# Kernel tuning notes

Measured on AMD Instinct MI355X. Metric: run time of the kernel, lower is better.

The kernel has to match this reference:

```python
import jax, jax.numpy as jnp
import numpy as np

N = 8192          # total proposals
D_IN = 256 * 7 * 7  # 12544
HID = 1024
C = 3


def setup_inputs() -> dict:
    key = jax.random.key(0)
    ks = jax.random.split(key, 9)
    s_in = 1.0 / np.sqrt(D_IN)
    s_h = 1.0 / np.sqrt(HID)
    return {
        "feature_vectors": jax.random.normal(ks[0], (N, D_IN), dtype=jnp.float32),
        "W1": jax.random.uniform(ks[1], (D_IN, HID), jnp.float32, -s_in, s_in),
        "b1": jax.random.uniform(ks[2], (HID,), jnp.float32, -s_in, s_in),
        "W2": jax.random.uniform(ks[3], (HID, HID), jnp.float32, -s_h, s_h),
        "b2": jax.random.uniform(ks[4], (HID,), jnp.float32, -s_h, s_h),
        "Wc": jax.random.uniform(ks[5], (HID, C + 1), jnp.float32, -s_h, s_h),
        "bc": jax.random.uniform(ks[6], (C + 1,), jnp.float32, -s_h, s_h),
        "Wr": jax.random.uniform(ks[7], (HID, 4 * C), jnp.float32, -s_h, s_h),
        "br": jax.random.uniform(ks[8], (4 * C,), jnp.float32, -s_h, s_h),
    }


def reference(feature_vectors, W1, b1, W2, b2, Wc, bc, Wr, br):
    # intermediate: Linear -> Linear -> ReLU (note: no ReLU between the two Linears,
    # matching the original nn.Sequential ordering)
    h = feature_vectors @ W1 + b1          # [N, 1024]
    h = h @ W2 + b2                        # [N, 1024]
    h = jax.nn.relu(h)
    class_logits = jax.nn.softmax(h @ Wc + bc, axis=-1)  # [N, C+1]
    box_pred = h @ Wr + br                  # [N, 4C]
    return class_logits, box_pred
```

## Files before the change

kernel.cpp:

```cpp
#include <hip/hip_runtime.h>
#include <hip/hip_bf16.h>
#include <stdint.h>

using u16 = unsigned short;
using u32 = unsigned int;

typedef __attribute__((ext_vector_type(8))) short short8;
typedef __attribute__((ext_vector_type(4))) float floatx4;

__device__ __forceinline__ u16 f2bf(float f) {
  __hip_bfloat16 h = __float2bfloat16(f);
  return *reinterpret_cast<u16*>(&h);
}

__device__ __forceinline__ void gl_lds16(const void* g, void* l) {
  __builtin_amdgcn_global_load_lds((const __attribute__((address_space(1))) void*)g,
                                   (__attribute__((address_space(3))) void*)l, 16, 0, 0);
}

__global__ __launch_bounds__(256)
void transpose_to_bf16(const float* __restrict__ in, u16* __restrict__ out,
                       int R, int Cc) {
  __shared__ float tile[32][33];
  int c0 = blockIdx.x * 32;
  int r0 = blockIdx.y * 32;
  int tx = threadIdx.x;
  int ty = threadIdx.y;
#pragma unroll
  for (int i = 0; i < 32; i += 8)
    tile[ty + i][tx] = in[(size_t)(r0 + ty + i) * Cc + c0 + tx];
  __syncthreads();
#pragma unroll
  for (int i = 0; i < 32; i += 8)
    out[(size_t)(c0 + ty + i) * R + r0 + tx] = f2bf(tile[tx][ty + i]);
}

__global__ __launch_bounds__(256)
void cvt_bf16(const float4* __restrict__ in, uint2* __restrict__ out, int n4) {
  int i = blockIdx.x * 256 + threadIdx.x;
  if (i >= n4) return;
  float4 v = in[i];
  u32 lo = (u32)f2bf(v.x) | ((u32)f2bf(v.y) << 16);
  u32 hi = (u32)f2bf(v.z) | ((u32)f2bf(v.w) << 16);
  out[i] = make_uint2(lo, hi);
}

constexpr int BM = 128, BN = 128, BK = 32;

template <bool A_BF16, bool RELU>
__global__ __launch_bounds__(256, 3)
void gemm_bt(const void* __restrict__ Aip, const u16* __restrict__ BT,
             const float* __restrict__ bias, u16* __restrict__ C,
             int M, int N, int K) {
  __shared__ __align__(16) u16 As[BM * BK];
  __shared__ __align__(16) u16 Bs[BN * BK];
  const int tid  = threadIdx.x;
  const int lane = tid & 63;
  const int wave = tid >> 6;
  const int m0 = blockIdx.y * BM;
  const int n0 = blockIdx.x * BN;
  const int wm = (wave & 1) * 64;
  const int wn = (wave >> 1) * 64;
  const int row = lane & 15;
  const int kq  = lane >> 4;

  floatx4 acc[4][4] = {};

  int a_off[4], b_off[4];
#pragma unroll
  for (int t = 0; t < 4; ++t) {
    int mr = wm + t * 16 + row;
    a_off[t] = mr * BK + ((kq ^ ((mr >> 1) & 3)) * 8);
    int nr = wn + t * 16 + row;
    b_off[t] = nr * BK + ((kq ^ ((nr >> 1) & 3)) * 8);
  }

  const u16* bptr[2];
  int b_lds[2];
#pragma unroll
  for (int it = 0; it < 2; ++it) {
    int c = it * 256 + tid;
    int nrow = c >> 2;
    int kc = ((c & 3) ^ ((nrow >> 1) & 3)) * 8;
    bptr[it] = BT + (size_t)(n0 + nrow) * K + kc;
    b_lds[it] = (it * 256 + wave * 64) * 8;
  }

  const u16* aptrB[2];
  int a_ldsB[2];
  const float* aptrF[4];
  int a_stF[4];
  if constexpr (A_BF16) {
    const u16* A = (const u16*)Aip;
#pragma unroll
    for (int it = 0; it < 2; ++it) {
      int c = it * 256 + tid;
      int mrow = c >> 2;
      int kc = ((c & 3) ^ ((mrow >> 1) & 3)) * 8;
      aptrB[it] = A + (size_t)(m0 + mrow) * K + kc;
      a_ldsB[it] = (it * 256 + wave * 64) * 8;
    }
  } else {
    const float* A = (const float*)Aip;
#pragma unroll
    for (int it = 0; it < 4; ++it) {
      int idx = it * 256 + tid;
      int mrow = idx >> 3;
      int kc = (idx & 7) * 4;
      aptrF[it] = A + (size_t)(m0 + mrow) * K + kc;
      int chunk = kc >> 3, half = (kc >> 2) & 1;
      int sc = chunk ^ ((mrow >> 1) & 3);
      a_stF[it] = mrow * BK + sc * 8 + half * 4;
    }
  }

  for (int k0 = 0; k0 < K; k0 += BK) {
    __syncthreads();
    if constexpr (A_BF16) {
#pragma unroll
      for (int it = 0; it < 2; ++it)
        gl_lds16(aptrB[it] + k0, &As[a_ldsB[it]]);
    } else {
#pragma unroll
      for (int it = 0; it < 4; ++it) {
        float4 v = *(const float4*)(aptrF[it] + k0);
        u32 lo = (u32)f2bf(v.x) | ((u32)f2bf(v.y) << 16);
        u32 hi = (u32)f2bf(v.z) | ((u32)f2bf(v.w) << 16);
        *(uint2*)&As[a_stF[it]] = make_uint2(lo, hi);
      }
    }
#pragma unroll
    for (int it = 0; it < 2; ++it)
      gl_lds16(bptr[it] + k0, &Bs[b_lds[it]]);
    __syncthreads();

    short8 a[4], b[4];
#pragma unroll
    for (int t = 0; t < 4; ++t) {
      a[t] = *(const short8*)&As[a_off[t]];
      b[t] = *(const short8*)&Bs[b_off[t]];
    }
#pragma unroll
    for (int mt = 0; mt < 4; ++mt)
#pragma unroll
      for (int nt = 0; nt < 4; ++nt)
        acc[mt][nt] = __builtin_amdgcn_mfma_f32_16x16x32_bf16(
            a[mt], b[nt], acc[mt][nt], 0, 0, 0);
  }

  const int ccol = row;
  const int crow = kq * 4;
#pragma unroll
  for (int mt = 0; mt < 4; ++mt) {
#pragma unroll
    for (int nt = 0; nt < 4; ++nt) {
      int gm = m0 + wm + mt * 16 + crow;
      int gn = n0 + wn + nt * 16 + ccol;
      float bv = bias[gn];
#pragma unroll
      for (int r = 0; r < 4; ++r) {
        float v = acc[mt][nt][r] + bv;
        if (RELU) v = fmaxf(v, 0.f);
        C[(size_t)(gm + r) * N + gn] = f2bf(v);
      }
    }
  }
}

constexpr int A_BUF  = 256 * 64;
constexpr int B_BUF  = 128 * 64;
constexpr int B_BASE = 3 * A_BUF;
constexpr int LDS_BYTES = (3 * A_BUF + 3 * B_BUF) * 2;

#define MM(i, j, va, vb) \
  acc[i][j] = __builtin_amdgcn_mfma_f32_16x16x32_bf16(va, vb, acc[i][j], 0, 0, 0)
#define MEMF() asm volatile("" ::: "memory")
#define BAR() do { MEMF(); __builtin_amdgcn_s_barrier(); MEMF(); } while (0)
#define STAGE_AH(h, bufo) \
  do { gl_lds16(apt[h][0], lds + (bufo) + adst[h][0]); apt[h][0] += 64; \
       gl_lds16(apt[h][1], lds + (bufo) + adst[h][1]); apt[h][1] += 64; } while (0)
#define STAGE_BH(h, bufo) \
  do { gl_lds16(bpt[h], lds + (bufo) + bdst[h]); bpt[h] += 64; } while (0)

template <bool RELU>
__global__ __launch_bounds__(512, 2)
void gemm256(const u16* __restrict__ A, const u16* __restrict__ BT,
             const float* __restrict__ bias, u16* __restrict__ C,
             int N, int K) {
  extern __shared__ u16 lds[];
  const int tid  = threadIdx.x;
  const int lane = tid & 63;
  const int wave = tid >> 6;
  const int wm = wave >> 1;
  const int wn = wave & 1;
  const int row = lane & 15;
  const int kq  = lane >> 4;
  const int sw  = lane & 7;

  const int orig = blockIdx.y * 8 + blockIdx.x;
  const int rr = ((orig & 7) << 5) | (orig >> 3);
  const int n0 = (rr & 7) * 128;
  const int m0 = (rr >> 3) * 256;

  const int o0 = ((kq) ^ sw) * 8;
  const int o1 = ((4 | kq) ^ sw) * 8;
  const int ar0 = (wm * 64 + row) * 64;
  const int ar1 = ar0 + 16 * 64;
  const int ar2 = ar0 + 32 * 64;
  const int ar3 = ar0 + 48 * 64;
  const int br0 = (wn * 64 + row) * 64;
  const int br1 = br0 + 16 * 64;
  const int br2 = br0 + 32 * 64;
  const int br3 = br0 + 48 * 64;

  const u16* apt[2][2];
  int adst[2][2];
#pragma unroll
  for (int h = 0; h < 2; ++h)
#pragma unroll
    for (int L = 0; L < 2; ++L) {
      int i = L * 512 + tid;
      int rg = h * 128 + (i >> 3);
      int c = i & 7;
      apt[h][L] = A + (size_t)(m0 + rg) * K + ((c ^ (rg & 7)) * 8);
      adst[h][L] = h * 8192 + L * 4096 + wave * 512;
    }
  const u16* bpt[2];
  int bdst[2];
#pragma unroll
  for (int h = 0; h < 2; ++h) {
    int rg = h * 64 + (tid >> 3);
    int c = tid & 7;
    bpt[h] = BT + (size_t)(n0 + rg) * K + ((c ^ (rg & 7)) * 8);
    bdst[h] = B_BASE + h * 4096 + wave * 512;
  }

  STAGE_AH(0, 0);      STAGE_AH(1, 0);      STAGE_BH(0, 0);     STAGE_BH(1, 0);
  STAGE_AH(0, A_BUF);  STAGE_AH(1, A_BUF);  STAGE_BH(0, B_BUF); STAGE_BH(1, B_BUF);
  asm volatile("s_waitcnt vmcnt(6)" ::: "memory");
  BAR();

  floatx4 acc[4][4] = {};
  int cb = 0, sb = 2;
  const int NT = K >> 6;
  for (int T = 0; T < NT; ++T) {
    const bool st = (T + 2 < NT);
    const u16* Ac = lds + cb * A_BUF;
    const u16* Bc = lds + B_BASE + cb * B_BUF;
    const int sA = sb * A_BUF;
    const int sB = sb * B_BUF;

    short8 a0k0, a0k1, a1k0, a1k1, a2k0, a2k1, a3k0, a3k1;
    short8 b0k0, b0k1, b1k0, b1k1, b2k0, b2k1, b3k0, b3k1;

    a0k0 = *(const short8*)(Ac + ar0 + o0);
    a0k1 = *(const short8*)(Ac + ar0 + o1);
    a1k0 = *(const short8*)(Ac + ar1 + o0);
    a1k1 = *(const short8*)(Ac + ar1 + o1);
    b0k0 = *(const short8*)(Bc + br0 + o0);
    b0k1 = *(const short8*)(Bc + br0 + o1);
    b1k0 = *(const short8*)(Bc + br1 + o0);
    b1k1 = *(const short8*)(Bc + br1 + o1);
    if (st) STAGE_AH(0, sA);
    BAR();
    __builtin_amdgcn_s_setprio(1);
    MM(0, 0, a0k0, b0k0); MM(0, 1, a0k0, b1k0);
    MM(1, 0, a1k0, b0k0); MM(1, 1, a1k0, b1k0);
    MM(0, 0, a0k1, b0k1); MM(0, 1, a0k1, b1k1);
    MM(1, 0, a1k1, b0k1); MM(1, 1, a1k1, b1k1);
    __builtin_amdgcn_s_setprio(0);
    BAR();

    b2k0 = *(const short8*)(Bc + br2 + o0);
    b2k1 = *(const short8*)(Bc + br2 + o1);
    b3k0 = *(const short8*)(Bc + br3 + o0);
    b3k1 = *(const short8*)(Bc + br3 + o1);
    if (st) STAGE_AH(1, sA);
    BAR();
    __builtin_amdgcn_s_setprio(1);
    MM(0, 2, a0k0, b2k0); MM(0, 3, a0k0, b3k0);
    MM(1, 2, a1k0, b2k0); MM(1, 3, a1k0, b3k0);
    MM(0, 2, a0k1, b2k1); MM(0, 3, a0k1, b3k1);
    MM(1, 2, a1k1, b2k1); MM(1, 3, a1k1, b3k1);
    __builtin_amdgcn_s_setprio(0);
    BAR();

    a2k0 = *(const short8*)(Ac + ar2 + o0);
    a2k1 = *(const short8*)(Ac + ar2 + o1);
    a3k0 = *(const short8*)(Ac + ar3 + o0);
    a3k1 = *(const short8*)(Ac + ar3 + o1);
    if (st) STAGE_BH(0, sB);
    BAR();
    __builtin_amdgcn_s_setprio(1);
    MM(2, 2, a2k0, b2k0); MM(2, 3, a2k0, b3k0);
    MM(3, 2, a3k0, b2k0); MM(3, 3, a3k0, b3k0);
    MM(2, 2, a2k1, b2k1); MM(2, 3, a2k1, b3k1);
    MM(3, 2, a3k1, b2k1); MM(3, 3, a3k1, b3k1);
    __builtin_amdgcn_s_setprio(0);
    BAR();

    if (st) STAGE_BH(1, sB);
    BAR();
    __builtin_amdgcn_s_setprio(1);
    MM(2, 0, a2k0, b0k0); MM(2, 1, a2k0, b1k0);
    MM(3, 0, a3k0, b0k0); MM(3, 1, a3k0, b1k0);
    MM(2, 0, a2k1, b0k1); MM(2, 1, a2k1, b1k1);
    MM(3, 0, a3k1, b0k1); MM(3, 1, a3k1, b1k1);
    __builtin_amdgcn_s_setprio(0);
    if (st) asm volatile("s_waitcnt vmcnt(6)" ::: "memory");
    else    asm volatile("s_waitcnt vmcnt(0)" ::: "memory");
    BAR();

    cb = (cb == 2) ? 0 : cb + 1;
    sb = (sb == 2) ? 0 : sb + 1;
  }

#pragma unroll
  for (int mt = 0; mt < 4; ++mt) {
#pragma unroll
    for (int nt = 0; nt < 4; ++nt) {
      int gm = m0 + wm * 64 + mt * 16 + kq * 4;
      int gn = n0 + wn * 64 + nt * 16 + row;
      float bv = bias[gn];
#pragma unroll
      for (int r = 0; r < 4; ++r) {
        float v = acc[mt][nt][r] + bv;
        if (RELU) v = fmaxf(v, 0.f);
        C[(size_t)(gm + r) * N + gn] = f2bf(v);
      }
    }
  }
}

__device__ __forceinline__ float wave_sum(float v) {
#pragma unroll
  for (int m = 32; m >= 1; m >>= 1) v += __shfl_xor(v, m, 64);
  return v;
}

__global__ __launch_bounds__(64)
void head_kernel(const u16* __restrict__ H, const float* __restrict__ Wc,
                 const float* __restrict__ bc, const float* __restrict__ Wr,
                 const float* __restrict__ br, float* __restrict__ out) {
  const int rowi = blockIdx.x;
  const int lane = threadIdx.x;
  const u16* h = H + (size_t)rowi * 1024 + lane * 16;
  uint4 p0 = *(const uint4*)h;
  uint4 p1 = *(const uint4*)(h + 8);
  u32 w[8] = {p0.x, p0.y, p0.z, p0.w, p1.x, p1.y, p1.z, p1.w};
  float x[16];
#pragma unroll
  for (int i = 0; i < 8; ++i) {
    union { u32 u; float f; } lo, hi;
    lo.u = w[i] << 16;
    hi.u = w[i] & 0xffff0000u;
    x[2 * i] = lo.f;
    x[2 * i + 1] = hi.f;
  }
  float ac[4] = {};
  float ar[12] = {};
  const int kbase = lane * 16;
#pragma unroll
  for (int j = 0; j < 16; ++j) {
    float xv = x[j];
    const float* wc = Wc + (size_t)(kbase + j) * 4;
#pragma unroll
    for (int c = 0; c < 4; ++c) ac[c] = fmaf(xv, wc[c], ac[c]);
    const float* wr = Wr + (size_t)(kbase + j) * 12;
#pragma unroll
    for (int r = 0; r < 12; ++r) ar[r] = fmaf(xv, wr[r], ar[r]);
  }
#pragma unroll
  for (int c = 0; c < 4; ++c) ac[c] = wave_sum(ac[c]);
#pragma unroll
  for (int r = 0; r < 12; ++r) ar[r] = wave_sum(ar[r]);

  if (lane == 0) {
    float lg[4], mx = -1e30f;
#pragma unroll
    for (int c = 0; c < 4; ++c) { lg[c] = ac[c] + bc[c]; mx = fmaxf(mx, lg[c]); }
    float s = 0.f;
#pragma unroll
    for (int c = 0; c < 4; ++c) { lg[c] = __expf(lg[c] - mx); s += lg[c]; }
    float inv = 1.f / s;
#pragma unroll
    for (int c = 0; c < 4; ++c) out[(size_t)rowi * 4 + c] = lg[c] * inv;
    float* ob = out + 8192 * 4;
#pragma unroll
    for (int r = 0; r < 12; ++r) ob[(size_t)rowi * 12 + r] = ar[r] + br[r];
  }
}

extern "C" void kernel_launch(void* const* d_in, const int* in_sizes, int n_in,
                              void* d_out, int out_size, void* d_ws, size_t ws_size,
                              hipStream_t stream) {
  const float* X  = (const float*)d_in[0];
  const float* W1 = (const float*)d_in[1];
  const float* b1 = (const float*)d_in[2];
  const float* W2 = (const float*)d_in[3];
  const float* b2 = (const float*)d_in[4];
  const float* Wc = (const float*)d_in[5];
  const float* bc = (const float*)d_in[6];
  const float* Wr = (const float*)d_in[7];
  const float* br = (const float*)d_in[8];

  constexpr int NP = 8192, DIN = 12544, HID = 1024;
  char* ws = (char*)d_ws;
  u16* W1T = (u16*)ws;
  u16* W2T = (u16*)(ws + (size_t)HID * DIN * 2);
  u16* H1  = (u16*)((char*)W2T + (size_t)HID * HID * 2);
  u16* Hb  = H1 + (size_t)NP * HID;
  u16* Xb  = Hb + (size_t)NP * HID;
  size_t need_base = (size_t)HID * DIN * 2 + (size_t)HID * HID * 2 +
                     2 * (size_t)NP * HID * 2;
  bool use_xbf = ws_size >= need_base + (size_t)NP * DIN * 2;

  static bool s_attr = false;
  if (!s_attr) {
    hipFuncSetAttribute(reinterpret_cast<const void*>(gemm256<false>),
                        hipFuncAttributeMaxDynamicSharedMemorySize, LDS_BYTES);
    hipFuncSetAttribute(reinterpret_cast<const void*>(gemm256<true>),
                        hipFuncAttributeMaxDynamicSharedMemorySize, LDS_BYTES);
    s_attr = true;
  }

  transpose_to_bf16<<<dim3(HID / 32, DIN / 32), dim3(32, 8), 0, stream>>>(W1, W1T, DIN, HID);
  transpose_to_bf16<<<dim3(HID / 32, HID / 32), dim3(32, 8), 0, stream>>>(W2, W2T, HID, HID);

  if (use_xbf) {
    int n4 = NP * DIN / 4;
    cvt_bf16<<<(n4 + 255) / 256, 256, 0, stream>>>((const float4*)X, (uint2*)Xb, n4);
    gemm256<false><<<dim3(8, NP / 256), 512, LDS_BYTES, stream>>>(
        Xb, W1T, b1, H1, HID, DIN);
  } else {
    gemm_bt<false, false><<<dim3(HID / BN, NP / BM), 256, 0, stream>>>(
        X, W1T, b1, H1, NP, HID, DIN);
  }
  gemm256<true><<<dim3(8, NP / 256), 512, LDS_BYTES, stream>>>(
      H1, W2T, b2, Hb, HID, HID);
  head_kernel<<<NP, 64, 0, stream>>>(Hb, Wc, bc, Wr, br, (float*)d_out);
}
```

Measured before the change: 877.1 us.

## Fuse fp32-to-bf16 conversion of X into first GEMM's load pipeline

Replaces the separate cvt_bf16 pass over X plus the bf16 GEMM with a new 256x128-tile kernel that loads fp32 X through registers, converts it to bf16 and writes it into double-buffered LDS while MFMAs run. This removes a full write and re-read of the 8192x12544 bf16 copy of X. The cost is that the A operand now goes through registers instead of direct global-to-LDS loads, and the kernel uses two LDS stages instead of three. The head kernel also packs four rows per 256-thread block to cut the block count.

```diff
diff --git a/kernel.cpp b/kernel.cpp
--- a/kernel.cpp
+++ b/kernel.cpp
@@ -35,147 +35,16 @@
     out[(size_t)(c0 + ty + i) * R + r0 + tx] = f2bf(tile[tx][ty + i]);
 }
 
-__global__ __launch_bounds__(256)
-void cvt_bf16(const float4* __restrict__ in, uint2* __restrict__ out, int n4) {
-  int i = blockIdx.x * 256 + threadIdx.x;
-  if (i >= n4) return;
-  float4 v = in[i];
-  u32 lo = (u32)f2bf(v.x) | ((u32)f2bf(v.y) << 16);
-  u32 hi = (u32)f2bf(v.z) | ((u32)f2bf(v.w) << 16);
-  out[i] = make_uint2(lo, hi);
-}
-
-constexpr int BM = 128, BN = 128, BK = 32;
-
-template <bool A_BF16, bool RELU>
-__global__ __launch_bounds__(256, 3)
-void gemm_bt(const void* __restrict__ Aip, const u16* __restrict__ BT,
-             const float* __restrict__ bias, u16* __restrict__ C,
-             int M, int N, int K) {
-  __shared__ __align__(16) u16 As[BM * BK];
-  __shared__ __align__(16) u16 Bs[BN * BK];
-  const int tid  = threadIdx.x;
-  const int lane = tid & 63;
-  const int wave = tid >> 6;
-  const int m0 = blockIdx.y * BM;
-  const int n0 = blockIdx.x * BN;
-  const int wm = (wave & 1) * 64;
-  const int wn = (wave >> 1) * 64;
-  const int row = lane & 15;
-  const int kq  = lane >> 4;
-
-  floatx4 acc[4][4] = {};
-
-  int a_off[4], b_off[4];
-#pragma unroll
-  for (int t = 0; t < 4; ++t) {
-    int mr = wm + t * 16 + row;
-    a_off[t] = mr * BK + ((kq ^ ((mr >> 1) & 3)) * 8);
-    int nr = wn + t * 16 + row;
-    b_off[t] = nr * BK + ((kq ^ ((nr >> 1) & 3)) * 8);
-  }
-
-  const u16* bptr[2];
-  int b_lds[2];
-#pragma unroll
-  for (int it = 0; it < 2; ++it) {
-    int c = it * 256 + tid;
-    int nrow = c >> 2;
-    int kc = ((c & 3) ^ ((nrow >> 1) & 3)) * 8;
-    bptr[it] = BT + (size_t)(n0 + nrow) * K + kc;
-    b_lds[it] = (it * 256 + wave * 64) * 8;
-  }
-
-  const u16* aptrB[2];
-  int a_ldsB[2];
-  const float* aptrF[4];
-  int a_stF[4];
-  if constexpr (A_BF16) {
-    const u16* A = (const u16*)Aip;
-#pragma unroll
-    for (int it = 0; it < 2; ++it) {
-      int c = it * 256 + tid;
-      int mrow = c >> 2;
-      int kc = ((c & 3) ^ ((mrow >> 1) & 3)) * 8;
-      aptrB[it] = A + (size_t)(m0 + mrow) * K + kc;
-      a_ldsB[it] = (it * 256 + wave * 64) * 8;
-    }
-  } else {
-    const float* A = (const float*)Aip;
-#pragma unroll
-    for (int it = 0; it < 4; ++it) {
-      int idx = it * 256 + tid;
-      int mrow = idx >> 3;
-      int kc = (idx & 7) * 4;
-      aptrF[it] = A + (size_t)(m0 + mrow) * K + kc;
-      int chunk = kc >> 3, half = (kc >> 2) & 1;
-      int sc = chunk ^ ((mrow >> 1) & 3);
-      a_stF[it] = mrow * BK + sc * 8 + half * 4;
-    }
-  }
-
-  for (int k0 = 0; k0 < K; k0 += BK) {
-    __syncthreads();
-    if constexpr (A_BF16) {
-#pragma unroll
-      for (int it = 0; it < 2; ++it)
-        gl_lds16(aptrB[it] + k0, &As[a_ldsB[it]]);
-    } else {
-#pragma unroll
-      for (int it = 0; it < 4; ++it) {
-        float4 v = *(const float4*)(aptrF[it] + k0);
-        u32 lo = (u32)f2bf(v.x) | ((u32)f2bf(v.y) << 16);
-        u32 hi = (u32)f2bf(v.z) | ((u32)f2bf(v.w) << 16);
-        *(uint2*)&As[a_stF[it]] = make_uint2(lo, hi);
-      }
-    }
-#pragma unroll
-    for (int it = 0; it < 2; ++it)
-      gl_lds16(bptr[it] + k0, &Bs[b_lds[it]]);
-    __syncthreads();
-
-    short8 a[4], b[4];
-#pragma unroll
-    for (int t = 0; t < 4; ++t) {
-      a[t] = *(const short8*)&As[a_off[t]];
-      b[t] = *(const short8*)&Bs[b_off[t]];
-    }
-#pragma unroll
-    for (int mt = 0; mt < 4; ++mt)
-#pragma unroll
-      for (int nt = 0; nt < 4; ++nt)
-        acc[mt][nt] = __builtin_amdgcn_mfma_f32_16x16x32_bf16(
-            a[mt], b[nt], acc[mt][nt], 0, 0, 0);
-  }
-
-  const int ccol = row;
-  const int crow = kq * 4;
-#pragma unroll
-  for (int mt = 0; mt < 4; ++mt) {
-#pragma unroll
-    for (int nt = 0; nt < 4; ++nt) {
-      int gm = m0 + wm + mt * 16 + crow;
-      int gn = n0 + wn + nt * 16 + ccol;
-      float bv = bias[gn];
-#pragma unroll
-      for (int r = 0; r < 4; ++r) {
-        float v = acc[mt][nt][r] + bv;
-        if (RELU) v = fmaxf(v, 0.f);
-        C[(size_t)(gm + r) * N + gn] = f2bf(v);
-      }
-    }
-  }
-}
+#define MM(i, j, va, vb) \
+  acc[i][j] = __builtin_amdgcn_mfma_f32_16x16x32_bf16(va, vb, acc[i][j], 0, 0, 0)
+#define MEMF() asm volatile("" ::: "memory")
+#define BAR() do { MEMF(); __builtin_amdgcn_s_barrier(); MEMF(); } while (0)
 
 constexpr int A_BUF  = 256 * 64;
 constexpr int B_BUF  = 128 * 64;
 constexpr int B_BASE = 3 * A_BUF;
 constexpr int LDS_BYTES = (3 * A_BUF + 3 * B_BUF) * 2;
 
-#define MM(i, j, va, vb) \
-  acc[i][j] = __builtin_amdgcn_mfma_f32_16x16x32_bf16(va, vb, acc[i][j], 0, 0, 0)
-#define MEMF() asm volatile("" ::: "memory")
-#define BAR() do { MEMF(); __builtin_amdgcn_s_barrier(); MEMF(); } while (0)
 #define STAGE_AH(h, bufo) \
   do { gl_lds16(apt[h][0], lds + (bufo) + adst[h][0]); apt[h][0] += 64; \
        gl_lds16(apt[h][1], lds + (bufo) + adst[h][1]); apt[h][1] += 64; } while (0)
@@ -332,18 +201,194 @@
   }
 }
 
+constexpr int FA_BUF  = 256 * 64;
+constexpr int FB_BUF  = 128 * 64;
+constexpr int FB_BASE = 2 * FA_BUF;
+constexpr int LDS_BYTES_F = (2 * FA_BUF + 2 * FB_BUF) * 2;
+
+__device__ __forceinline__ void cvtw64(u16* dst, float4 v) {
+  u32 lo = (u32)f2bf(v.x) | ((u32)f2bf(v.y) << 16);
+  u32 hi = (u32)f2bf(v.z) | ((u32)f2bf(v.w) << 16);
+  *(uint2*)dst = make_uint2(lo, hi);
+}
+
+__global__ __launch_bounds__(512, 2)
+void gemm256F(const float* __restrict__ A, const u16* __restrict__ BT,
+              const float* __restrict__ bias, u16* __restrict__ C,
+              int N, int K) {
+  extern __shared__ u16 lds[];
+  const int tid  = threadIdx.x;
+  const int lane = tid & 63;
+  const int wave = tid >> 6;
+  const int wm = wave >> 1;
+  const int wn = wave & 1;
+  const int row = lane & 15;
+  const int kq  = lane >> 4;
+  const int sw  = lane & 7;
+
+  const int orig = blockIdx.y * 8 + blockIdx.x;
+  const int rr = ((orig & 7) << 5) | (orig >> 3);
+  const int n0 = (rr & 7) * 128;
+  const int m0 = (rr >> 3) * 256;
+
+  const int o0 = ((kq) ^ sw) * 8;
+  const int o1 = ((4 | kq) ^ sw) * 8;
+  const int ar0 = (wm * 64 + row) * 64;
+  const int ar1 = ar0 + 16 * 64;
+  const int ar2 = ar0 + 32 * 64;
+  const int ar3 = ar0 + 48 * 64;
+  const int br0 = (wn * 64 + row) * 64;
+  const int br1 = br0 + 16 * 64;
+  const int br2 = br0 + 32 * 64;
+  const int br3 = br0 + 48 * 64;
+
+  const u16* bpt[2];
+  int bdst[2];
+#pragma unroll
+  for (int h = 0; h < 2; ++h) {
+    int rg = h * 64 + (tid >> 3);
+    int c = tid & 7;
+    bpt[h] = BT + (size_t)(n0 + rg) * K + ((c ^ (rg & 7)) * 8);
+    bdst[h] = h * 4096 + wave * 512;
+  }
+
+  const float* aFk = A + (size_t)(m0 + (tid >> 4)) * K + (tid & 15) * 4;
+  const int r0t = tid >> 4;
+  const int c4 = tid & 15;
+  const int adst0 = r0t * 64 + (((c4 >> 1) ^ (r0t & 7)) * 8) + (c4 & 1) * 4;
+
+  float4 rA[2][4];
+
+#define FSTAGE_ISSUE(nB_)                                              \
+  do {                                                                 \
+    MEMF();                                                            \
+    gl_lds16(bpt[0], lds + (nB_) + bdst[0]); bpt[0] += 64;             \
+    gl_lds16(bpt[1], lds + (nB_) + bdst[1]); bpt[1] += 64;             \
+    MEMF();                                                            \
+    _Pragma("unroll")                                                  \
+    for (int h = 0; h < 2; ++h)                                        \
+      _Pragma("unroll")                                                \
+      for (int i = 0; i < 4; ++i)                                      \
+        rA[h][i] = *(const float4*)(aFk + (size_t)(h * 128 + i * 32) * K); \
+    aFk += 64;                                                         \
+    MEMF();                                                            \
+  } while (0)
+
+#define FSTAGE_WRITE(nA_)                                              \
+  do {                                                                 \
+    asm volatile("s_waitcnt vmcnt(4)" ::: "memory");                   \
+    _Pragma("unroll")                                                  \
+    for (int i = 0; i < 4; ++i)                                        \
+      cvtw64(lds + (nA_) + adst0 + (i * 32) * 64, rA[0][i]);           \
+    asm volatile("s_waitcnt vmcnt(0)" ::: "memory");                   \
+    _Pragma("unroll")                                                  \
+    for (int i = 0; i < 4; ++i)                                        \
+      cvtw64(lds + (nA_) + adst0 + ((128 + i * 32)) * 64, rA[1][i]);   \
+  } while (0)
+
+  FSTAGE_ISSUE(FB_BASE + 0);
+  FSTAGE_WRITE(0);
+  asm volatile("s_waitcnt lgkmcnt(0)" ::: "memory");
+  BAR();
+
+  floatx4 acc[4][4] = {};
+  const int NT = K >> 6;
+  for (int T = 0; T < NT; ++T) {
+    const int cur = T & 1;
+    const bool st = (T + 1 < NT);
+    const u16* Ac = lds + cur * FA_BUF;
+    const u16* Bc = lds + FB_BASE + cur * FB_BUF;
+    const int nA = (cur ^ 1) * FA_BUF;
+    const int nB = FB_BASE + (cur ^ 1) * FB_BUF;
+
+    short8 a0k0, a0k1, a1k0, a1k1, a2k0, a2k1, a3k0, a3k1;
+    short8 b0k0, b0k1, b1k0, b1k1, b2k0, b2k1, b3k0, b3k1;
+
+    a0k0 = *(const short8*)(Ac + ar0 + o0);
+    a0k1 = *(const short8*)(Ac + ar0 + o1);
+    a1k0 = *(const short8*)(Ac + ar1 + o0);
+    a1k1 = *(const short8*)(Ac + ar1 + o1);
+    b0k0 = *(const short8*)(Bc + br0 + o0);
+    b0k1 = *(const short8*)(Bc + br0 + o1);
+    b1k0 = *(const short8*)(Bc + br1 + o0);
+    b1k1 = *(const short8*)(Bc + br1 + o1);
+    if (st) FSTAGE_ISSUE(nB);
+    BAR();
+    __builtin_amdgcn_s_setprio(1);
+    MM(0, 0, a0k0, b0k0); MM(0, 1, a0k0, b1k0);
+    MM(1, 0, a1k0, b0k0); MM(1, 1, a1k0, b1k0);
+    MM(0, 0, a0k1, b0k1); MM(0, 1, a0k1, b1k1);
+    MM(1, 0, a1k1, b0k1); MM(1, 1, a1k1, b1k1);
+    __builtin_amdgcn_s_setprio(0);
+    BAR();
+
+    b2k0 = *(const short8*)(Bc + br2 + o0);
+    b2k1 = *(const short8*)(Bc + br2 + o1);
+    b3k0 = *(const short8*)(Bc + br3 + o0);
+    b3k1 = *(const short8*)(Bc + br3 + o1);
+    BAR();
+    __builtin_amdgcn_s_setprio(1);
+    MM(0, 2, a0k0, b2k0); MM(0, 3, a0k0, b3k0);
+    MM(1, 2, a1k0, b2k0); MM(1, 3, a1k0, b3k0);
+    MM(0, 2, a0k1, b2k1); MM(0, 3, a0k1, b3k1);
+    MM(1, 2, a1k1, b2k1); MM(1, 3, a1k1, b3k1);
+    __builtin_amdgcn_s_setprio(0);
+    BAR();
+
+    a2k0 = *(const short8*)(Ac + ar2 + o0);
+    a2k1 = *(const short8*)(Ac + ar2 + o1);
+    a3k0 = *(const short8*)(Ac + ar3 + o0);
+    a3k1 = *(const short8*)(Ac + ar3 + o1);
+    BAR();
+    __builtin_amdgcn_s_setprio(1);
+    MM(2, 2, a2k0, b2k0); MM(2, 3, a2k0, b3k0);
+    MM(3, 2, a3k0, b2k0); MM(3, 3, a3k0, b3k0);
+    MM(2, 2, a2k1, b2k1); MM(2, 3, a2k1, b3k1);
+    MM(3, 2, a3k1, b2k1); MM(3, 3, a3k1, b3k1);
+    __builtin_amdgcn_s_setprio(0);
+    BAR();
+
+    if (st) FSTAGE_WRITE(nA);
+    __builtin_amdgcn_s_setprio(1);
+    MM(2, 0, a2k0, b0k0); MM(2, 1, a2k0, b1k0);
+    MM(3, 0, a3k0, b0k0); MM(3, 1, a3k0, b1k0);
+    MM(2, 0, a2k1, b0k1); MM(2, 1, a2k1, b1k1);
+    MM(3, 0, a3k1, b0k1); MM(3, 1, a3k1, b1k1);
+    __builtin_amdgcn_s_setprio(0);
+    asm volatile("s_waitcnt lgkmcnt(0)" ::: "memory");
+    BAR();
+  }
+
+#pragma unroll
+  for (int mt = 0; mt < 4; ++mt) {
+#pragma unroll
+    for (int nt = 0; nt < 4; ++nt) {
+      int gm = m0 + wm * 64 + mt * 16 + kq * 4;
+      int gn = n0 + wn * 64 + nt * 16 + row;
+      float bv = bias[gn];
+#pragma unroll
+      for (int r = 0; r < 4; ++r) {
+        float v = acc[mt][nt][r] + bv;
+        C[(size_t)(gm + r) * N + gn] = f2bf(v);
+      }
+    }
+  }
+#undef FSTAGE_ISSUE
+#undef FSTAGE_WRITE
+}
+
 __device__ __forceinline__ float wave_sum(float v) {
 #pragma unroll
   for (int m = 32; m >= 1; m >>= 1) v += __shfl_xor(v, m, 64);
   return v;
 }
 
-__global__ __launch_bounds__(64)
+__global__ __launch_bounds__(256)
 void head_kernel(const u16* __restrict__ H, const float* __restrict__ Wc,
                  const float* __restrict__ bc, const float* __restrict__ Wr,
                  const float* __restrict__ br, float* __restrict__ out) {
-  const int rowi = blockIdx.x;
-  const int lane = threadIdx.x;
+  const int rowi = blockIdx.x * 4 + (threadIdx.x >> 6);
+  const int lane = threadIdx.x & 63;
   const u16* h = H + (size_t)rowi * 1024 + lane * 16;
   uint4 p0 = *(const uint4*)h;
   uint4 p1 = *(const uint4*)(h + 8);
@@ -410,15 +455,12 @@
   u16* W2T = (u16*)(ws + (size_t)HID * DIN * 2);
   u16* H1  = (u16*)((char*)W2T + (size_t)HID * HID * 2);
   u16* Hb  = H1 + (size_t)NP * HID;
-  u16* Xb  = Hb + (size_t)NP * HID;
-  size_t need_base = (size_t)HID * DIN * 2 + (size_t)HID * HID * 2 +
-                     2 * (size_t)NP * HID * 2;
-  bool use_xbf = ws_size >= need_base + (size_t)NP * DIN * 2;
+  (void)ws_size;
 
   static bool s_attr = false;
   if (!s_attr) {
-    hipFuncSetAttribute(reinterpret_cast<const void*>(gemm256<false>),
-                        hipFuncAttributeMaxDynamicSharedMemorySize, LDS_BYTES);
+    hipFuncSetAttribute(reinterpret_cast<const void*>(gemm256F),
+                        hipFuncAttributeMaxDynamicSharedMemorySize, LDS_BYTES_F);
     hipFuncSetAttribute(reinterpret_cast<const void*>(gemm256<true>),
                         hipFuncAttributeMaxDynamicSharedMemorySize, LDS_BYTES);
     s_attr = true;
@@ -427,16 +469,9 @@
   transpose_to_bf16<<<dim3(HID / 32, DIN / 32), dim3(32, 8), 0, stream>>>(W1, W1T, DIN, HID);
   transpose_to_bf16<<<dim3(HID / 32, HID / 32), dim3(32, 8), 0, stream>>>(W2, W2T, HID, HID);
 
-  if (use_xbf) {
-    int n4 = NP * DIN / 4;
-    cvt_bf16<<<(n4 + 255) / 256, 256, 0, stream>>>((const float4*)X, (uint2*)Xb, n4);
-    gemm256<false><<<dim3(8, NP / 256), 512, LDS_BYTES, stream>>>(
-        Xb, W1T, b1, H1, HID, DIN);
-  } else {
-    gemm_bt<false, false><<<dim3(HID / BN, NP / BM), 256, 0, stream>>>(
-        X, W1T, b1, H1, NP, HID, DIN);
-  }
+  gemm256F<<<dim3(8, NP / 256), 512, LDS_BYTES_F, stream>>>(
+      X, W1T, b1, H1, HID, DIN);
   gemm256<true><<<dim3(8, NP / 256), 512, LDS_BYTES, stream>>>(
       H1, W2T, b2, Hb, HID, HID);
-  head_kernel<<<NP, 64, 0, stream>>>(Hb, Wc, bc, Wr, br, (float*)d_out);
-}
+  head_kernel<<<NP / 4, 256, 0, stream>>>(Hb, Wc, bc, Wr, br, (float*)d_out);
+}
```

After: 1.070 ms. 1.22x slower.
